# Optimization experiments

Measured on AMD Instinct MI355X. Metric: run time of the kernel, lower is better.

Reference implementation:

```python
import jax, jax.numpy as jnp
import numpy as np

T, B, D = 1024, 32, 256
TRACE, CTX, OUT = 64, 16, 256


def setup_inputs() -> dict:
    key = jax.random.key(0)
    ks = jax.random.split(key, 12)
    x = jax.random.normal(ks[0], (T, B, D), dtype=jnp.float32)
    start = jax.random.randint(ks[1], (T, B), 0, 2).astype(bool)
    state_re = jnp.zeros((B, TRACE, CTX), dtype=jnp.float32)
    state_im = jnp.zeros((B, TRACE, CTX), dtype=jnp.float32)
    s = 0.02
    w_gate_in = s * jax.random.normal(ks[2], (D, TRACE), dtype=jnp.float32)
    b_gate_in = jnp.zeros((TRACE,), jnp.float32)
    w_pre = s * jax.random.normal(ks[3], (D, TRACE), dtype=jnp.float32)
    b_pre = jnp.zeros((TRACE,), jnp.float32)
    w_z = s * jax.random.normal(ks[4], (2 * TRACE * CTX, OUT), dtype=jnp.float32)
    b_z = jnp.zeros((OUT,), jnp.float32)
    w_gate_out = s * jax.random.normal(ks[5], (D, OUT), dtype=jnp.float32)
    b_gate_out = jnp.zeros((OUT,), jnp.float32)
    w_skip = s * jax.random.normal(ks[6], (D, OUT), dtype=jnp.float32)
    b_skip = jnp.zeros((OUT,), jnp.float32)
    # deterministic FFM params per init_deterministic_a/b
    ffm_a = jnp.linspace(1e-6, 0.5, TRACE).astype(jnp.float32)
    ffm_b = (2 * jnp.pi / jnp.linspace(1.0, 1000.0, CTX)).astype(jnp.float32)
    return dict(x=x, start=start, state_re=state_re, state_im=state_im,
                w_gate_in=w_gate_in, b_gate_in=b_gate_in, w_pre=w_pre, b_pre=b_pre,
                w_z=w_z, b_z=b_z, w_gate_out=w_gate_out, b_gate_out=b_gate_out,
                w_skip=w_skip, b_skip=b_skip, ffm_a=ffm_a, ffm_b=ffm_b)


def _layer_norm(y, eps=1e-6):
    mu = jnp.mean(y, axis=-1, keepdims=True)
    var = jnp.mean(jnp.square(y - mu), axis=-1, keepdims=True)
    return (y - mu) / jnp.sqrt(var + eps)


def _ffm_forward(x, start, state_re, state_im, w_gate_in, b_gate_in, w_pre, b_pre,
                 w_z, b_z, w_gate_out, b_gate_out, w_skip, b_skip, ffm_a, ffm_b):
    Tn, Bn = x.shape[0], x.shape[1]
    # map_to_h
    gate_in = jax.nn.sigmoid(x @ w_gate_in + b_gate_in)           # [T,B,trace]
    gated = (x @ w_pre + b_pre) * gate_in                          # [T,B,trace]
    scan_in = jnp.broadcast_to(gated[..., None], (Tn, Bn, TRACE, CTX)).astype(jnp.complex64)
    # log_gamma decay matrix ab: [1,1,trace,ctx] complex
    a = -jnp.abs(ffm_a).reshape(1, 1, TRACE, 1)
    b = ffm_b.reshape(1, 1, 1, CTX)
    ab = jax.lax.complex(jnp.broadcast_to(a, (1, 1, TRACE, CTX)),
                         jnp.broadcast_to(b, (1, 1, TRACE, CTX)))
    # scan: prepend initial state, reset-aware associative update
    state0 = jax.lax.complex(state_re, state_im)[None]             # [1,B,trace,ctx]
    xs = jnp.concatenate([state0, scan_in], axis=0)                # [T+1,B,trace,ctx]
    st = jnp.concatenate([jnp.zeros((1, Bn, 1, 1), bool),
                          start.reshape(Tn, Bn, 1, 1)], axis=0)    # [T+1,B,1,1]
    ts = jnp.ones((Tn + 1, Bn, 1, 1), dtype=jnp.float32)

    def update(carry, incoming):
        prev_start, s, i = carry
        stt, xx, j = incoming
        keep = jnp.logical_not(stt)
        s = s * keep
        j = j * keep
        s = s * jnp.exp(ab * j) + xx
        return (jnp.logical_or(stt, prev_start), s, j + i)

    _, new_state, _ = jax.lax.associative_scan(update, (st, xs, ts), axis=0)
    state = new_state[1:]                                          # [T,B,trace,ctx]
    # map_from_h
    z_in = jnp.concatenate([jnp.real(state), jnp.imag(state)], axis=-1).reshape(Tn, Bn, -1)
    z = z_in @ w_z + b_z                                           # [T,B,out]
    gate_out = jax.nn.sigmoid(x @ w_gate_out + b_gate_out)
    skip = x @ w_skip + b_skip
    out = _layer_norm(z * gate_out) + skip * (1.0 - gate_out)
    final_state = state[-1]                                        # [B,trace,ctx]
    return final_state, out


def reference(x, start, state_re, state_im, w_gate_in, b_gate_in, w_pre, b_pre,
              w_z, b_z, w_gate_out, b_gate_out, w_skip, b_skip, ffm_a, ffm_b):
    return _ffm_forward(x, start, state_re, state_im, w_gate_in, b_gate_in,
                        w_pre, b_pre, w_z, b_z, w_gate_out, b_gate_out,
                        w_skip, b_skip, ffm_a, ffm_b)
```

## Files before the change

### kernel.cpp

```cpp
#include <hip/hip_runtime.h>
#include <hip/hip_bf16.h>

#define T_DIM 1024
#define B_DIM 32
#define D_DIM 256
#define TRACE 64
#define CTX 16
#define OUT_DIM 256
#define TB (T_DIM * B_DIM)
#define KZ (2 * TRACE * CTX)
#define NP 640
#define NCH 8
#define CHL 128

typedef short short8 __attribute__((ext_vector_type(8)));
typedef float floatx4 __attribute__((ext_vector_type(4)));
typedef unsigned short ushortx4 __attribute__((ext_vector_type(4)));

__device__ __forceinline__ float bf2f(unsigned short u) {
  return __uint_as_float((unsigned int)u << 16);
}
__device__ __forceinline__ float sigm(float v) {
  return 1.f / (1.f + expf(-v));
}
__device__ __forceinline__ void gload_lds16(const void* g, void* l) {
  __builtin_amdgcn_global_load_lds(
      (const __attribute__((address_space(1))) void*)g,
      (__attribute__((address_space(3))) void*)l, 16, 0, 0);
}

__global__ __launch_bounds__(256) void k_prep_all(
    const unsigned char* __restrict__ s, int* __restrict__ startw,
    const float* __restrict__ wz, __hip_bfloat16* __restrict__ wzt,
    const float* __restrict__ wgi, const float* __restrict__ bgi,
    const float* __restrict__ wpr, const float* __restrict__ bpr,
    const float* __restrict__ wgo, const float* __restrict__ bgo,
    const float* __restrict__ wsk, const float* __restrict__ bsk,
    __hip_bfloat16* __restrict__ wcat, float* __restrict__ bcat,
    const float* __restrict__ x, __hip_bfloat16* __restrict__ xb) {
  const int bid = blockIdx.x;
  const int tid = threadIdx.x;
  if (bid >= 896) {
    size_t i = ((size_t)(bid - 896) * 256 + tid) * 8;
    float4 a = *reinterpret_cast<const float4*>(x + i);
    float4 b = *reinterpret_cast<const float4*>(x + i + 4);
    unsigned short u[8];
    u[0] = __bfloat16_as_ushort(__float2bfloat16(a.x));
    u[1] = __bfloat16_as_ushort(__float2bfloat16(a.y));
    u[2] = __bfloat16_as_ushort(__float2bfloat16(a.z));
    u[3] = __bfloat16_as_ushort(__float2bfloat16(a.w));
    u[4] = __bfloat16_as_ushort(__float2bfloat16(b.x));
    u[5] = __bfloat16_as_ushort(__float2bfloat16(b.y));
    u[6] = __bfloat16_as_ushort(__float2bfloat16(b.z));
    u[7] = __bfloat16_as_ushort(__float2bfloat16(b.w));
    *reinterpret_cast<uint4*>(xb + i) = *reinterpret_cast<uint4*>(u);
    return;
  }
  if (bid < 128) {
    __shared__ int a1, a3, a4;
    if (tid == 0) { a1 = 0; a3 = 0; a4 = 0; }
    __syncthreads();
    int l1 = 0, l3 = 0, l4 = 0;
    for (int i = tid; i < 32768; i += 256) {
      unsigned char v = s[i];
      if (v) {
        if ((i & 3) == 1) l1 = 1;
        if ((i & 3) == 3) l3 = 1;
        if ((i & 7) == 4) l4 = 1;
      }
    }
    if (l1) atomicOr(&a1, 1);
    if (l3) atomicOr(&a3, 1);
    if (l4) atomicOr(&a4, 1);
    __syncthreads();
    int f = a1 ? 1 : (a3 ? 2 : (a4 ? 0 : 3));
    int i = bid * 256 + tid;
    int v;
    if (f == 1)      v = s[i] != 0;
    else if (f == 2) v = reinterpret_cast<const float*>(s)[i] != 0.f;
    else if (f == 3) v = reinterpret_cast<const long long*>(s)[i] != 0;
    else             v = reinterpret_cast<const int*>(s)[i] != 0;
    startw[i] = v;
  } else if (bid < 256) {
    const int t = bid - 128;
    const int tk = t & 31;
    const int tn = t >> 5;
    const int k0 = tk * 64, n0 = tn * 64;
    __shared__ float sm[64][65];
    for (int i = tid; i < 4096; i += 256) {
      int r = i >> 6, c = i & 63;
      sm[r][c] = wz[(size_t)(k0 + r) * 256 + n0 + c];
    }
    __syncthreads();
    for (int i = tid; i < 4096; i += 256) {
      int r = i >> 6, c = i & 63;
      int src = (c & 0x20) | ((c & 1) << 4) | ((c >> 1) & 15);
      wzt[(size_t)(n0 + r) * 2048 + k0 + c] = __float2bfloat16(sm[src][r]);
    }
  } else {
    const int n = bid - 256, k = tid;
    float v, bv;
    if (n < 64)        { v = wgi[k * 64 + n];          bv = bgi[n]; }
    else if (n < 128)  { v = wpr[k * 64 + (n - 64)];   bv = bpr[n - 64]; }
    else if (n < 384)  { v = wgo[k * 256 + (n - 128)]; bv = bgo[n - 128]; }
    else               { v = wsk[k * 256 + (n - 384)]; bv = bsk[n - 384]; }
    wcat[(size_t)n * 256 + k] = __float2bfloat16(v);
    if (k == 0) bcat[n] = bv;
  }
}

__global__ __launch_bounds__(256) void k_gemm_xproj(
    const __hip_bfloat16* __restrict__ A, const __hip_bfloat16* __restrict__ Bm,
    const float* __restrict__ bias, __hip_bfloat16* __restrict__ C) {
  int wg = (blockIdx.x & 7) * 160 + (blockIdx.x >> 3);
  const int n0 = (wg % 5) * 128;
  const int r0 = (wg / 5) * 128;
  const int tid = threadIdx.x;
  const int l = tid & 63;
  const int wid = tid >> 6;
  const int wr = wid >> 1;
  const int wc = wid & 1;

  __shared__ __align__(16) char ldsA[16384];
  __shared__ __align__(16) char ldsB[16384];

  floatx4 acc[4][4];
#pragma unroll
  for (int m = 0; m < 4; ++m)
#pragma unroll
    for (int n = 0; n < 4; ++n) acc[m][n] = (floatx4)0.f;

  int aoff[4][2], boff[4][2];
#pragma unroll
  for (int m = 0; m < 4; ++m) {
    int row = wr * 64 + m * 16 + (l & 15);
#pragma unroll
    for (int ks = 0; ks < 2; ++ks) {
      int byte = row * 128 + ks * 64 + (l >> 4) * 16;
      aoff[m][ks] = byte ^ ((row & 7) << 4);
    }
    int col = wc * 64 + m * 16 + (l & 15);
#pragma unroll
    for (int ks = 0; ks < 2; ++ks) {
      int byte = col * 128 + ks * 64 + (l >> 4) * 16;
      boff[m][ks] = byte ^ ((col & 7) << 4);
    }
  }

  for (int kt = 0; kt < 256; kt += 64) {
#pragma unroll
    for (int i = 0; i < 4; ++i) {
      int c = tid + i * 256;
      int row = c >> 3;
      int kgs = (c & 7) ^ (row & 7);
      gload_lds16(A + (size_t)(r0 + row) * 256 + kt + kgs * 8,
                  ldsA + i * 4096 + wid * 1024);
      gload_lds16(Bm + (size_t)(n0 + row) * 256 + kt + kgs * 8,
                  ldsB + i * 4096 + wid * 1024);
    }
    __syncthreads();
#pragma unroll
    for (int ks = 0; ks < 2; ++ks) {
      short8 a[4], b[4];
#pragma unroll
      for (int m = 0; m < 4; ++m)
        a[m] = *reinterpret_cast<const short8*>(ldsA + aoff[m][ks]);
#pragma unroll
      for (int n = 0; n < 4; ++n)
        b[n] = *reinterpret_cast<const short8*>(ldsB + boff[n][ks]);
#pragma unroll
      for (int m = 0; m < 4; ++m)
#pragma unroll
        for (int n = 0; n < 4; ++n)
          acc[m][n] = __builtin_amdgcn_mfma_f32_16x16x32_bf16(
              a[m], b[n], acc[m][n], 0, 0, 0);
    }
    __syncthreads();
  }

#pragma unroll
  for (int m = 0; m < 4; ++m) {
#pragma unroll
    for (int n = 0; n < 4; ++n) {
      int gc = n0 + wc * 64 + n * 16 + (l & 15);
      float bzv = bias[gc];
      bool dosig = (gc < 64) || (gc >= 128 && gc < 384);
#pragma unroll
      for (int j = 0; j < 4; ++j) {
        int gr = r0 + wr * 64 + m * 16 + (l >> 4) * 4 + j;
        float v = acc[m][n][j] + bzv;
        if (dosig) v = sigm(v);
        C[(size_t)gr * NP + gc] = __float2bfloat16(v);
      }
    }
  }
}

__global__ __launch_bounds__(256, 2) void k_zgemm_ln(
    const __hip_bfloat16* __restrict__ zin, const __hip_bfloat16* __restrict__ wzt,
    const float* __restrict__ bz, const __hip_bfloat16* __restrict__ proj,
    float* __restrict__ out) {
  const int r0 = blockIdx.x * 64;
  const int tid = threadIdx.x;
  const int l = tid & 63;
  const int w = tid >> 6;

  __shared__ __align__(16) char lds[81920];
  float* red1 = (float*)lds;
  float* red2 = (float*)(lds + 1024);

  floatx4 acc[4][4];
#pragma unroll
  for (int m = 0; m < 4; ++m)
#pragma unroll
    for (int n = 0; n < 4; ++n) acc[m][n] = (floatx4)0.f;

  int aoff[4][2], boff[4][2];
#pragma unroll
  for (int m = 0; m < 4; ++m) {
    int row = m * 16 + (l & 15);
#pragma unroll
    for (int ks = 0; ks < 2; ++ks) {
      int byte = row * 128 + ks * 64 + (l >> 4) * 16;
      aoff[m][ks] = byte ^ ((row & 7) << 4);
    }
  }
#pragma unroll
  for (int n = 0; n < 4; ++n) {
    int col = w * 64 + n * 16 + (l & 15);
#pragma unroll
    for (int ks = 0; ks < 2; ++ks) {
      int byte = col * 128 + ks * 64 + (l >> 4) * 16;
      boff[n][ks] = byte ^ ((col & 7) << 4);
    }
  }

  auto STAGE = [&](int kt, int sel) {
    char* pA = lds + (sel ? 8192 : 0);
    char* pB = lds + 16384 + (sel ? 32768 : 0);
#pragma unroll
    for (int i = 0; i < 2; ++i) {
      int c = tid + i * 256;
      int row = c >> 3;
      int kgs = (c & 7) ^ (row & 7);
      gload_lds16(zin + (size_t)(r0 + row) * KZ + kt + kgs * 8,
                  pA + i * 4096 + w * 1024);
    }
#pragma unroll
    for (int i = 0; i < 8; ++i) {
      int c = tid + i * 256;
      int row = c >> 3;
      int kgs = (c & 7) ^ (row & 7);
      gload_lds16(wzt + (size_t)row * KZ + kt + kgs * 8,
                  pB + i * 4096 + w * 1024);
    }
  };
  auto COMPUTE = [&](int sel) {
    const char* pA = lds + (sel ? 8192 : 0);
    const char* pB = lds + 16384 + (sel ? 32768 : 0);
#pragma unroll
    for (int ks = 0; ks < 2; ++ks) {
      short8 a[4], b[4];
#pragma unroll
      for (int m = 0; m < 4; ++m)
        a[m] = *reinterpret_cast<const short8*>(pA + aoff[m][ks]);
#pragma unroll
      for (int n = 0; n < 4; ++n)
        b[n] = *reinterpret_cast<const short8*>(pB + boff[n][ks]);
#pragma unroll
      for (int m = 0; m < 4; ++m)
#pragma unroll
        for (int n = 0; n < 4; ++n)
          acc[m][n] = __builtin_amdgcn_mfma_f32_16x16x32_bf16(
              a[m], b[n], acc[m][n], 0, 0, 0);
    }
  };

  STAGE(0, 0);
  asm volatile("s_waitcnt vmcnt(0)" ::: "memory");
  __builtin_amdgcn_s_barrier();
  for (int t = 0; t < 31; ++t) {
    STAGE((t + 1) * 64, (t + 1) & 1);
    COMPUTE(t & 1);
    asm volatile("s_waitcnt vmcnt(0)" ::: "memory");
    __builtin_amdgcn_s_barrier();
  }
  COMPUTE(1);

  float bzv[4];
#pragma unroll
  for (int n = 0; n < 4; ++n) bzv[n] = bz[w * 64 + n * 16 + (l & 15)];

  float q[4][4][4];
#pragma unroll
  for (int m = 0; m < 4; ++m) {
#pragma unroll
    for (int j = 0; j < 4; ++j) {
      int row = m * 16 + (l >> 4) * 4 + j;
      const __hip_bfloat16* prow = proj + (size_t)(r0 + row) * NP;
      float s1 = 0.f, s2 = 0.f;
#pragma unroll
      for (int n = 0; n < 4; ++n) {
        int col = w * 64 + n * 16 + (l & 15);
        float go = __bfloat162float(prow[128 + col]);
        float ps = __bfloat162float(prow[384 + col]);
        float y = (acc[m][n][j] + bzv[n]) * go;
        acc[m][n][j] = y;
        q[m][n][j] = ps * (1.f - go);
        s1 += y;
        s2 += y * y;
      }
#pragma unroll
      for (int off = 8; off > 0; off >>= 1) {
        s1 += __shfl_xor(s1, off);
        s2 += __shfl_xor(s2, off);
      }
      if ((l & 15) == 0) { red1[row * 4 + w] = s1; red2[row * 4 + w] = s2; }
    }
  }
  __syncthreads();

#pragma unroll
  for (int m = 0; m < 4; ++m) {
#pragma unroll
    for (int j = 0; j < 4; ++j) {
      int row = m * 16 + (l >> 4) * 4 + j;
      int gr = r0 + row;
      float t1 = red1[row * 4 + 0] + red1[row * 4 + 1] +
                 red1[row * 4 + 2] + red1[row * 4 + 3];
      float t2 = red2[row * 4 + 0] + red2[row * 4 + 1] +
                 red2[row * 4 + 2] + red2[row * 4 + 3];
      float mu = t1 * (1.f / 256.f);
      float var = t2 * (1.f / 256.f) - mu * mu;
      float rs = rsqrtf(var + 1e-6f);
#pragma unroll
      for (int n = 0; n < 4; ++n) {
        int col = w * 64 + n * 16 + (l & 15);
        out[(size_t)gr * 256 + col] = (acc[m][n][j] - mu) * rs + q[m][n][j];
      }
    }
  }
}

__global__ __launch_bounds__(64) void k_scan_a(
    const __hip_bfloat16* __restrict__ proj, const int* __restrict__ startw,
    const float* __restrict__ ffm_a, const float* __restrict__ ffm_b,
    float2* __restrict__ carry, int* __restrict__ rstflag) {
  const int c  = blockIdx.x >> 9;
  const int bb = (blockIdx.x >> 4) & 31;
  const int tg = blockIdx.x & 15;
  const int tid = threadIdx.x;
  const int tl = tid >> 4, cx = tid & 15;
  const int trace = tg * 4 + tl;
  const int t0 = c * CHL;
  __shared__ float gs[CHL * 4];
  __shared__ int ss[CHL];
  for (int t = tid; t < CHL; t += 64) {
    size_t base = ((size_t)(t0 + t) * B_DIM + bb) * NP + tg * 4;
    ushortx4 pg4 = *reinterpret_cast<const ushortx4*>(proj + base);
    ushortx4 pp4 = *reinterpret_cast<const ushortx4*>(proj + base + 64);
    float4 o;
    o.x = bf2f(pp4[0]) * bf2f(pg4[0]);
    o.y = bf2f(pp4[1]) * bf2f(pg4[1]);
    o.z = bf2f(pp4[2]) * bf2f(pg4[2]);
    o.w = bf2f(pp4[3]) * bf2f(pg4[3]);
    *reinterpret_cast<float4*>(&gs[t * 4]) = o;
    ss[t] = startw[(t0 + t) * B_DIM + bb];
  }
  __syncthreads();

  int lrst = ss[tid] | ss[tid + 64];
  int any = __any(lrst != 0);
  if (tid == 0 && tg == 0) rstflag[c * B_DIM + bb] = any;

  float decay = expf(-fabsf(ffm_a[trace]));
  float th = ffm_b[cx];
  float cr = decay * cosf(th);
  float ci = decay * sinf(th);
  float sr = 0.f, si = 0.f;
  for (int t = 0; t < CHL; ++t) {
    float g = gs[t * 4 + tl];
    int rst = ss[t];
    float nr = fmaf(sr, cr, fmaf(-si, ci, g));
    float ni = fmaf(sr, ci, si * cr);
    sr = rst ? g : nr;
    si = rst ? 0.f : ni;
  }
  carry[((size_t)(c * B_DIM + bb) * TRACE + trace) * CTX + cx] =
      make_float2(sr, si);
}

__global__ __launch_bounds__(64) void k_scan_c(
    const __hip_bfloat16* __restrict__ proj, const int* __restrict__ startw,
    const float* __restrict__ state_re, const float* __restrict__ state_im,
    const float* __restrict__ ffm_a, const float* __restrict__ ffm_b,
    const float2* __restrict__ carry, const int* __restrict__ rstflag,
    __hip_bfloat16* __restrict__ zin, float* __restrict__ fstate) {
  const int c  = blockIdx.x >> 9;
  const int bb = (blockIdx.x >> 4) & 31;
  const int tg = blockIdx.x & 15;
  const int tid = threadIdx.x;
  const int tl = tid >> 4, cx = tid & 15;
  const int trace = tg * 4 + tl;
  const int t0 = c * CHL;
  __shared__ float gs[CHL * 4];
  __shared__ int ss[CHL];
  for (int t = tid; t < CHL; t += 64) {
    size_t base = ((size_t)(t0 + t) * B_DIM + bb) * NP + tg * 4;
    ushortx4 pg4 = *reinterpret_cast<const ushortx4*>(proj + base);
    ushortx4 pp4 = *reinterpret_cast<const ushortx4*>(proj + base + 64);
    float4 o;
    o.x = bf2f(pp4[0]) * bf2f(pg4[0]);
    o.y = bf2f(pp4[1]) * bf2f(pg4[1]);
    o.z = bf2f(pp4[2]) * bf2f(pg4[2]);
    o.w = bf2f(pp4[3]) * bf2f(pg4[3]);
    *reinterpret_cast<float4*>(&gs[t * 4]) = o;
    ss[t] = startw[(t0 + t) * B_DIM + bb];
  }
  __syncthreads();

  float decay = expf(-fabsf(ffm_a[trace]));
  float th = ffm_b[cx];
  float cr = decay * cosf(th);
  float ci = decay * sinf(th);

  float pr = cr, pi = ci;
#pragma unroll
  for (int q = 0; q < 7; ++q) {
    float nr = pr * pr - pi * pi;
    float ni = 2.f * pr * pi;
    pr = nr; pi = ni;
  }

  const int chain = (bb * TRACE + trace) * CTX + cx;
  float sr = state_re[chain];
  float si = state_im[chain];
  for (int j = 0; j < c; ++j) {
    float2 cj = carry[((size_t)(j * B_DIM + bb) * TRACE + trace) * CTX + cx];
    if (rstflag[j * B_DIM + bb]) {
      sr = cj.x; si = cj.y;
    } else {
      float nsr = fmaf(pr, sr, fmaf(-pi, si, cj.x));
      float nsi = fmaf(pr, si, fmaf(pi, sr, cj.y));
      sr = nsr; si = nsi;
    }
  }

  const size_t zbase = (size_t)trace * 32 + cx * 2;
  for (int t = 0; t < CHL; ++t) {
    float g = gs[t * 4 + tl];
    int rst = ss[t];
    float nr = fmaf(sr, cr, fmaf(-si, ci, g));
    float ni = fmaf(sr, ci, si * cr);
    sr = rst ? g : nr;
    si = rst ? 0.f : ni;
    unsigned int u = (unsigned int)__bfloat16_as_ushort(__float2bfloat16(sr)) |
                     ((unsigned int)__bfloat16_as_ushort(__float2bfloat16(si)) << 16);
    *reinterpret_cast<unsigned int*>(
        zin + ((size_t)(t0 + t) * B_DIM + bb) * KZ + zbase) = u;
  }
  if (c == NCH - 1) fstate[chain] = sr;
}

extern "C" void kernel_launch(void* const* d_in, const int* in_sizes, int n_in,
                              void* d_out, int out_size, void* d_ws, size_t ws_size,
                              hipStream_t stream) {
  const float* x         = (const float*)d_in[0];
  const unsigned char* start_raw = (const unsigned char*)d_in[1];
  const float* state_re  = (const float*)d_in[2];
  const float* state_im  = (const float*)d_in[3];
  const float* w_gate_in = (const float*)d_in[4];
  const float* b_gate_in = (const float*)d_in[5];
  const float* w_pre     = (const float*)d_in[6];
  const float* b_pre     = (const float*)d_in[7];
  const float* w_z       = (const float*)d_in[8];
  const float* b_z       = (const float*)d_in[9];
  const float* w_gate_out= (const float*)d_in[10];
  const float* b_gate_out= (const float*)d_in[11];
  const float* w_skip    = (const float*)d_in[12];
  const float* b_skip    = (const float*)d_in[13];
  const float* ffm_a     = (const float*)d_in[14];
  const float* ffm_b     = (const float*)d_in[15];

  char* ws = (char*)d_ws;
  int* startw   = (int*)(ws + 4096);
  int* rstflag  = (int*)(ws + (132 << 10));
  float* bcat   = (float*)(ws + (160 << 10));
  __hip_bfloat16* wcat =
      (__hip_bfloat16*)(ws + (256 << 10));
  __hip_bfloat16* wzt =
      (__hip_bfloat16*)(ws + ((size_t)1 << 20));
  float2* carry = (float2*)(ws + ((size_t)2 << 20));
  __hip_bfloat16* proj =
      (__hip_bfloat16*)(ws + ((size_t)4 << 20));
  __hip_bfloat16* xb =
      (__hip_bfloat16*)(ws + ((size_t)44 << 20));
  __hip_bfloat16* zin =
      (__hip_bfloat16*)(ws + ((size_t)60 << 20));

  float* fstate = (float*)d_out;
  float* out    = (float*)d_out + B_DIM * TRACE * CTX;

  k_prep_all<<<896 + 4096, 256, 0, stream>>>(
      start_raw, startw, w_z, wzt,
      w_gate_in, b_gate_in, w_pre, b_pre,
      w_gate_out, b_gate_out, w_skip, b_skip,
      wcat, bcat, x, xb);
  k_gemm_xproj<<<1280, 256, 0, stream>>>(xb, wcat, bcat, proj);
  k_scan_a<<<(NCH - 1) * B_DIM * 16, 64, 0, stream>>>(
      proj, startw, ffm_a, ffm_b, carry, rstflag);
  k_scan_c<<<NCH * B_DIM * 16, 64, 0, stream>>>(
      proj, startw, state_re, state_im, ffm_a, ffm_b, carry, rstflag,
      zin, fstate);
  k_zgemm_ln<<<TB / 64, 256, 0, stream>>>(zin, wzt, b_z, proj, out);
}
```

Before: 174.4 us.

## Double scan chunk count and vectorize start-flag format detection in prep kernel

Splits the time scan into 16 chunks of 64 steps instead of 8 of 128, which doubles scan parallelism and shortens each block's serial recurrence. The chunk-power exponent drops to 2^6 and the carry buffer is enlarged by moving later workspace regions. The prep kernel is reordered so the x-to-bf16 conversion blocks come first. The start-flag format detection now reads the input as 16-byte words with bitmasks instead of a byte loop, and writes four flags per thread with 32 blocks instead of 128. The trade-off is a longer sequential carry-combine loop in the final scan pass.

```diff
diff --git a/kernel.cpp b/kernel.cpp
--- a/kernel.cpp
+++ b/kernel.cpp
@@ -10,8 +10,8 @@
 #define TB (T_DIM * B_DIM)
 #define KZ (2 * TRACE * CTX)
 #define NP 640
-#define NCH 8
-#define CHL 128
+#define NCH 16
+#define CHL 64
 
 typedef short short8 __attribute__((ext_vector_type(8)));
 typedef float floatx4 __attribute__((ext_vector_type(4)));
@@ -40,8 +40,8 @@
     const float* __restrict__ x, __hip_bfloat16* __restrict__ xb) {
   const int bid = blockIdx.x;
   const int tid = threadIdx.x;
-  if (bid >= 896) {
-    size_t i = ((size_t)(bid - 896) * 256 + tid) * 8;
+  if (bid < 4096) {
+    size_t i = ((size_t)bid * 256 + tid) * 8;
     float4 a = *reinterpret_cast<const float4*>(x + i);
     float4 b = *reinterpret_cast<const float4*>(x + i + 4);
     unsigned short u[8];
@@ -56,33 +56,44 @@
     *reinterpret_cast<uint4*>(xb + i) = *reinterpret_cast<uint4*>(u);
     return;
   }
-  if (bid < 128) {
-    __shared__ int a1, a3, a4;
-    if (tid == 0) { a1 = 0; a3 = 0; a4 = 0; }
+  if (bid < 4128) {
+    unsigned o1 = 0, o3 = 0, o4 = 0;
+    for (int i = tid; i < 2048; i += 256) {
+      uint4 wv = reinterpret_cast<const uint4*>(s)[i];
+      unsigned allw = wv.x | wv.y | wv.z | wv.w;
+      o1 |= allw & 0x0000FF00u;
+      o3 |= allw & 0xFF000000u;
+      o4 |= (wv.y | wv.w) & 0x000000FFu;
+    }
+    __shared__ unsigned s1, s3, s4;
+    if (tid == 0) { s1 = 0; s3 = 0; s4 = 0; }
     __syncthreads();
-    int l1 = 0, l3 = 0, l4 = 0;
-    for (int i = tid; i < 32768; i += 256) {
-      unsigned char v = s[i];
-      if (v) {
-        if ((i & 3) == 1) l1 = 1;
-        if ((i & 3) == 3) l3 = 1;
-        if ((i & 7) == 4) l4 = 1;
-      }
-    }
-    if (l1) atomicOr(&a1, 1);
-    if (l3) atomicOr(&a3, 1);
-    if (l4) atomicOr(&a4, 1);
+    if (o1) atomicOr(&s1, 1u);
+    if (o3) atomicOr(&s3, 1u);
+    if (o4) atomicOr(&s4, 1u);
     __syncthreads();
-    int f = a1 ? 1 : (a3 ? 2 : (a4 ? 0 : 3));
-    int i = bid * 256 + tid;
-    int v;
-    if (f == 1)      v = s[i] != 0;
-    else if (f == 2) v = reinterpret_cast<const float*>(s)[i] != 0.f;
-    else if (f == 3) v = reinterpret_cast<const long long*>(s)[i] != 0;
-    else             v = reinterpret_cast<const int*>(s)[i] != 0;
-    startw[i] = v;
-  } else if (bid < 256) {
-    const int t = bid - 128;
+    int f = s1 ? 1 : (s3 ? 2 : (s4 ? 0 : 3));
+    int base = (bid - 4096) * 1024 + tid * 4;
+    int4 v;
+    if (f == 1) {
+      uchar4 b4 = reinterpret_cast<const uchar4*>(s)[base >> 2];
+      v = make_int4(b4.x != 0, b4.y != 0, b4.z != 0, b4.w != 0);
+    } else if (f == 2) {
+      float4 fv = reinterpret_cast<const float4*>(s)[base >> 2];
+      v = make_int4(fv.x != 0.f, fv.y != 0.f, fv.z != 0.f, fv.w != 0.f);
+    } else if (f == 3) {
+      const long long* p = reinterpret_cast<const long long*>(s);
+      v = make_int4(p[base] != 0, p[base + 1] != 0,
+                    p[base + 2] != 0, p[base + 3] != 0);
+    } else {
+      int4 iv = reinterpret_cast<const int4*>(s)[base >> 2];
+      v = make_int4(iv.x != 0, iv.y != 0, iv.z != 0, iv.w != 0);
+    }
+    reinterpret_cast<int4*>(startw)[base >> 2] = v;
+    return;
+  }
+  if (bid < 4256) {
+    const int t = bid - 4128;
     const int tk = t & 31;
     const int tn = t >> 5;
     const int k0 = tk * 64, n0 = tn * 64;
@@ -97,16 +108,16 @@
       int src = (c & 0x20) | ((c & 1) << 4) | ((c >> 1) & 15);
       wzt[(size_t)(n0 + r) * 2048 + k0 + c] = __float2bfloat16(sm[src][r]);
     }
-  } else {
-    const int n = bid - 256, k = tid;
-    float v, bv;
-    if (n < 64)        { v = wgi[k * 64 + n];          bv = bgi[n]; }
-    else if (n < 128)  { v = wpr[k * 64 + (n - 64)];   bv = bpr[n - 64]; }
-    else if (n < 384)  { v = wgo[k * 256 + (n - 128)]; bv = bgo[n - 128]; }
-    else               { v = wsk[k * 256 + (n - 384)]; bv = bsk[n - 384]; }
-    wcat[(size_t)n * 256 + k] = __float2bfloat16(v);
-    if (k == 0) bcat[n] = bv;
-  }
+    return;
+  }
+  const int n = bid - 4256, k = tid;
+  float v, bv;
+  if (n < 64)        { v = wgi[k * 64 + n];          bv = bgi[n]; }
+  else if (n < 128)  { v = wpr[k * 64 + (n - 64)];   bv = bpr[n - 64]; }
+  else if (n < 384)  { v = wgo[k * 256 + (n - 128)]; bv = bgo[n - 128]; }
+  else               { v = wsk[k * 256 + (n - 384)]; bv = bsk[n - 384]; }
+  wcat[(size_t)n * 256 + k] = __float2bfloat16(v);
+  if (k == 0) bcat[n] = bv;
 }
 
 __global__ __launch_bounds__(256) void k_gemm_xproj(
@@ -369,8 +380,7 @@
   }
   __syncthreads();
 
-  int lrst = ss[tid] | ss[tid + 64];
-  int any = __any(lrst != 0);
+  int any = __any(ss[tid] != 0);
   if (tid == 0 && tg == 0) rstflag[c * B_DIM + bb] = any;
 
   float decay = expf(-fabsf(ffm_a[trace]));
@@ -426,7 +436,7 @@
 
   float pr = cr, pi = ci;
 #pragma unroll
-  for (int q = 0; q < 7; ++q) {
+  for (int q = 0; q < 6; ++q) {
     float nr = pr * pr - pi * pi;
     float ni = 2.f * pr * pi;
     pr = nr; pi = ni;
@@ -492,16 +502,16 @@
       (__hip_bfloat16*)(ws + ((size_t)1 << 20));
   float2* carry = (float2*)(ws + ((size_t)2 << 20));
   __hip_bfloat16* proj =
-      (__hip_bfloat16*)(ws + ((size_t)4 << 20));
+      (__hip_bfloat16*)(ws + ((size_t)6 << 20));
   __hip_bfloat16* xb =
-      (__hip_bfloat16*)(ws + ((size_t)44 << 20));
+      (__hip_bfloat16*)(ws + ((size_t)46 << 20));
   __hip_bfloat16* zin =
-      (__hip_bfloat16*)(ws + ((size_t)60 << 20));
+      (__hip_bfloat16*)(ws + ((size_t)62 << 20));
 
   float* fstate = (float*)d_out;
   float* out    = (float*)d_out + B_DIM * TRACE * CTX;
 
-  k_prep_all<<<896 + 4096, 256, 0, stream>>>(
+  k_prep_all<<<4896, 256, 0, stream>>>(
       start_raw, startw, w_z, wzt,
       w_gate_in, b_gate_in, w_pre, b_pre,
       w_gate_out, b_gate_out, w_skip, b_skip,
```

Result: faster. 146.2 us (-16.2%).
